# Kernel optimization log

Measured on AMD Instinct MI355X. Metric: run time of the kernel, lower is better.

The kernel has to match this reference:

```python
import jax, jax.numpy as jnp
import numpy as np

N, E, IN, HID, H, HD, PE_D, D, L = 50000, 800000, 128, 64, 4, 16, 16, 16, 2
BN_S = 1.0 / np.sqrt(1.0 + 1e-5)  # eval-mode BatchNorm1d with default running stats (mean=0, var=1)
SCALE = 1.0 / np.sqrt(HD)         # np.sqrt(self.out_dim) with out_dim = head_dim


def _ln(x, g, b, eps=1e-5):
    mu = jnp.mean(x, -1, keepdims=True)
    v = jnp.mean((x - mu) ** 2, -1, keepdims=True)
    return (x - mu) * jax.lax.rsqrt(v + eps) * g + b


def setup_inputs() -> dict:
    key = jax.random.key(0)
    ks = iter(jax.random.split(key, 64))

    def nrm(shape, s=0.05):
        return jax.random.normal(next(ks), shape, jnp.float32) * s

    return {
        'src': jax.random.randint(next(ks), (E,), 0, N),
        'dst': jnp.sort(jax.random.randint(next(ks), (E,), 0, N)),
        'x': nrm((N, IN), 1.0), 'pe': nrm((N, PE_D), 1.0),
        'de': nrm((E, D), 1.0), 'm': nrm((E, 8), 1.0), 'I': nrm((N, D), 1.0),
        'W_h': nrm((IN, HID)),
        'W_pe': nrm((PE_D, HID)), 'b_pe': jnp.zeros((HID,)),
        'W_de': nrm((D, HID)), 'b_de': jnp.zeros((HID,)),
        'W_m': nrm((8, HID)), 'b_m': jnp.zeros((HID,)),
        'Wq': nrm((L, HID, HID)), 'bq': jnp.zeros((L, HID)),
        'Wk': nrm((L, HID, HID)), 'bk': jnp.zeros((L, HID)),
        'Wv': nrm((L, HID, HID)), 'bv': jnp.zeros((L, HID)),
        'Wpd': nrm((L, HID, HID)), 'bpd': jnp.zeros((L, HID)),
        'Wpm': nrm((L, HID, HID)), 'bpm': jnp.zeros((L, HID)),
        'WO': nrm((L, HID, HID)), 'bO': jnp.zeros((L, HID)),
        'Wpi': nrm((L, D, HID)), 'bpi': jnp.zeros((L, HID)),
        'g1': jnp.ones((L, HID)), 'b1': jnp.zeros((L, HID)),
        'g2': jnp.ones((L, HID)), 'b2': jnp.zeros((L, HID)),
        'Wf1': nrm((L, HID, 2 * HID)), 'bf1': jnp.zeros((L, 2 * HID)),
        'Wf2': nrm((L, 2 * HID, HID)), 'bf2': jnp.zeros((L, HID)),
        'Wr1': nrm((HID, 16)), 'br1': jnp.zeros((16,)),
        'Wr2': nrm((16, IN)), 'br2': jnp.zeros((IN,)),
    }


def _forward(src, dst, x, pe, de, m, I, W_h, W_pe, b_pe, W_de, b_de, W_m, b_m,
             Wq, bq, Wk, bk, Wv, bv, Wpd, bpd, Wpm, bpm, WO, bO, Wpi, bpi,
             g1, b1, g2, b2, Wf1, bf1, Wf2, bf2, Wr1, br1, Wr2, br2):
    h = x @ W_h + pe @ W_pe + b_pe          # [N, HID]
    m_e = m @ W_m + b_m                     # [E, HID]
    de_e = de @ W_de + b_de                 # [E, HID]
    for l in range(L):
        h_in1 = h
        Qh = (h @ Wq[l] + bq[l]).reshape(N, H, HD)
        Kh = (h @ Wk[l] + bk[l]).reshape(N, H, HD)
        Vh = (h @ Wv[l] + bv[l]).reshape(N, H, HD)
        pd = (de_e @ Wpd[l] + bpd[l]).reshape(E, H, HD)
        pm = (m_e @ Wpm[l] + bpm[l]).reshape(E, H, HD)
        # edge scores: src_dot_dst -> scale -> + proj_d -> + proj_m -> exp(clamped sum)
        s = jnp.sum(Kh[src] * Qh[dst], -1, keepdims=True) * SCALE   # [E, H, 1]
        s = jnp.sum(s + pd + pm, -1, keepdims=True)                 # [E, H, 1]
        s = jnp.exp(jnp.clip(s, -5.0, 5.0))
        # scatter-sum message passing to destination nodes
        wV = jax.ops.segment_sum(Vh[src] * s, dst, num_segments=N, indices_are_sorted=True)
        z = jax.ops.segment_sum(s, dst, num_segments=N, indices_are_sorted=True)
        h = (wV / (z + 1e-10)).reshape(N, HID)
        h = h + I @ Wpi[l] + bpi[l]          # dropout is identity in eval
        h = h @ WO[l] + bO[l]
        h = h_in1 + h
        h = _ln(h, g1[l], b1[l]) * BN_S      # LayerNorm then eval BatchNorm
        h_in2 = h
        h2 = jax.nn.relu(h @ Wf1[l] + bf1[l]) @ Wf2[l] + bf2[l]
        h = _ln(h_in2 + h2, g2[l], b2[l]) * BN_S
    x_hat = jax.nn.selu(h @ Wr1 + br1) @ Wr2 + br2
    return h, x_hat


def reference(src, dst, x, pe, de, m, I, W_h, W_pe, b_pe, W_de, b_de, W_m, b_m,
              Wq, bq, Wk, bk, Wv, bv, Wpd, bpd, Wpm, bpm, WO, bO, Wpi, bpi,
              g1, b1, g2, b2, Wf1, bf1, Wf2, bf2, Wr1, br1, Wr2, br2):
    return _forward(src, dst, x, pe, de, m, I, W_h, W_pe, b_pe, W_de, b_de, W_m, b_m,
                    Wq, bq, Wk, bk, Wv, bv, Wpd, bpd, Wpm, bpm, WO, bO, Wpi, bpi,
                    g1, b1, g2, b2, Wf1, bf1, Wf2, bf2, Wr1, br1, Wr2, br2)
```

## Files before the change

### kernel.cpp

```cpp
#include <hip/hip_runtime.h>
#include <hip/hip_bf16.h>

typedef __hip_bfloat16 bf16;
typedef __attribute__((ext_vector_type(8))) short s8v;
typedef __attribute__((ext_vector_type(4))) float f4v;
typedef __attribute__((ext_vector_type(8))) _Float16 h8v;
#define DEV __device__ __forceinline__
#define MFMA(a, b, c) __builtin_amdgcn_mfma_f32_16x16x32_bf16(a, b, c, 0, 0, 0)

constexpr int OFF_WQ = 0, OFF_WK = 8192, OFF_WV = 16384, OFF_WO = 24576;
constexpr int OFF_WF1 = 32768, OFF_WF2 = 49152, OFF_WPI = 65536;
constexpr int PL = 69632;
constexpr int OFF_WH = 139264, OFF_WPE = 155648, OFF_WR1 = 159744, OFF_WR2 = 161792;
constexpr int WBF_TOT = 169984;

constexpr float LOG2E = 1.4426950408889634f;
constexpr float QSC = 4.f * LOG2E;
constexpr float CLB = 5.f * LOG2E;

DEV short f2bs(float f) { union { bf16 b; short s; } u; u.b = __float2bfloat16(f); return u.s; }
DEV float bs2f(short s) { union { bf16 b; short s2; } u; u.s2 = s; return __bfloat162float(u.b); }
DEV ushort f2hs(float f) { union { _Float16 h; ushort u; } x; x.h = (_Float16)f; return x.u; }

DEV void split8(const float* p, s8v& hi, s8v& lo) {
  #pragma unroll
  for (int j = 0; j < 8; ++j) {
    float f = p[j];
    short h = f2bs(f);
    hi[j] = h;
    lo[j] = f2bs(f - bs2f(h));
  }
}

__global__ __launch_bounds__(256) void prep_kernel(
    const float* __restrict__ Wq, const float* __restrict__ Wk,
    const float* __restrict__ Wv, const float* __restrict__ WO,
    const float* __restrict__ Wf1, const float* __restrict__ Wf2,
    const float* __restrict__ Wpi, const float* __restrict__ W_h,
    const float* __restrict__ W_pe, const float* __restrict__ Wr1,
    const float* __restrict__ Wr2, short* __restrict__ wb)
{
  const float* sp; int K, ksh, Nc, d0;
  switch (blockIdx.y) {
    case 0:  sp = Wq;         K = 64;  ksh = 6; Nc = 64;  d0 = OFF_WQ;       break;
    case 1:  sp = Wk;         K = 64;  ksh = 6; Nc = 64;  d0 = OFF_WK;       break;
    case 2:  sp = Wv;         K = 64;  ksh = 6; Nc = 64;  d0 = OFF_WV;       break;
    case 3:  sp = WO;         K = 64;  ksh = 6; Nc = 64;  d0 = OFF_WO;       break;
    case 4:  sp = Wf1;        K = 64;  ksh = 6; Nc = 128; d0 = OFF_WF1;      break;
    case 5:  sp = Wf2;        K = 128; ksh = 7; Nc = 64;  d0 = OFF_WF2;      break;
    case 6:  sp = Wpi;        K = 16;  ksh = 5; Nc = 64;  d0 = OFF_WPI;      break;
    case 7:  sp = Wq + 4096;  K = 64;  ksh = 6; Nc = 64;  d0 = PL + OFF_WQ;  break;
    case 8:  sp = Wk + 4096;  K = 64;  ksh = 6; Nc = 64;  d0 = PL + OFF_WK;  break;
    case 9:  sp = Wv + 4096;  K = 64;  ksh = 6; Nc = 64;  d0 = PL + OFF_WV;  break;
    case 10: sp = WO + 4096;  K = 64;  ksh = 6; Nc = 64;  d0 = PL + OFF_WO;  break;
    case 11: sp = Wf1 + 8192; K = 64;  ksh = 6; Nc = 128; d0 = PL + OFF_WF1; break;
    case 12: sp = Wf2 + 8192; K = 128; ksh = 7; Nc = 64;  d0 = PL + OFF_WF2; break;
    case 13: sp = Wpi + 1024; K = 16;  ksh = 5; Nc = 64;  d0 = PL + OFF_WPI; break;
    case 14: sp = W_h;        K = 128; ksh = 7; Nc = 64;  d0 = OFF_WH;       break;
    case 15: sp = W_pe;       K = 16;  ksh = 5; Nc = 64;  d0 = OFF_WPE;      break;
    case 16: sp = Wr1;        K = 64;  ksh = 6; Nc = 16;  d0 = OFF_WR1;      break;
    default: sp = Wr2;        K = 16;  ksh = 5; Nc = 128; d0 = OFF_WR2;      break;
  }
  int Kp = 1 << ksh;
  int tot = Kp * Nc;
  int i = blockIdx.x * 256 + threadIdx.x;
  if (i >= tot) return;
  int o = i >> ksh, kk = i & (Kp - 1);
  float v = (kk < K) ? sp[kk * Nc + o] : 0.f;
  short h = f2bs(v);
  wb[d0 + i] = h;
  wb[d0 + tot + i] = f2bs(v - bs2f(h));
}

__global__ __launch_bounds__(256) void fold_kernel(
    const float* __restrict__ W_de, const float* __restrict__ b_de,
    const float* __restrict__ W_m,  const float* __restrict__ b_m,
    const float* __restrict__ Wpd,  const float* __restrict__ bpd,
    const float* __restrict__ Wpm,  const float* __restrict__ bpm,
    float* __restrict__ fold)
{
  __shared__ float spd[64][4], spm[64][4];
  int tid = threadIdx.x;
  for (int l = 0; l < 2; ++l) {
    {
      int t = tid >> 2, hh = tid & 3;
      const float* wpd = Wpd + l * 4096 + t * 64 + hh * 16;
      const float* wpm = Wpm + l * 4096 + t * 64 + hh * 16;
      float sd = 0.f, sm = 0.f;
      #pragma unroll
      for (int hd = 0; hd < 16; ++hd) { sd += wpd[hd]; sm += wpm[hd]; }
      spd[t][hh] = sd; spm[t][hh] = sm;
    }
    __syncthreads();
    if (tid < 64) { int i = tid >> 2, hh = tid & 3;
      float a = 0.f;
      for (int k = 0; k < 64; ++k) a += W_de[i * 64 + k] * spd[k][hh];
      fold[l * 128 + i * 4 + hh] = a; }
    if (tid < 32) { int i = tid >> 2, hh = tid & 3;
      float a = 0.f;
      for (int k = 0; k < 64; ++k) a += W_m[i * 64 + k] * spm[k][hh];
      fold[l * 128 + 64 + i * 4 + hh] = a; }
    if (tid < 4) { int hh = tid;
      float a = 0.f;
      for (int k = 0; k < 64; ++k) a += b_de[k] * spd[k][hh] + b_m[k] * spm[k][hh];
      for (int hd = 0; hd < 16; ++hd)
        a += bpd[l * 64 + hh * 16 + hd] + bpm[l * 64 + hh * 16 + hd];
      fold[l * 128 + 96 + hh] = a; }
    __syncthreads();
  }
}

__global__ __launch_bounds__(256) void escore_kernel(
    const float* __restrict__ de, const float* __restrict__ m,
    const float* __restrict__ fold, ushort* __restrict__ ep0,
    ushort* __restrict__ ep1, int E, int lay)
{
  int e = blockIdx.x * 256 + threadIdx.x;
  if (e >= E) return;
  float dv[16], mv[8];
  #pragma unroll
  for (int i = 0; i < 4; ++i)
    *(float4*)(dv + 4 * i) = ((const float4*)(de + (size_t)e * 16))[i];
  #pragma unroll
  for (int i = 0; i < 2; ++i)
    *(float4*)(mv + 4 * i) = ((const float4*)(m + (size_t)e * 8))[i];
  #pragma unroll
  for (int pass = 0; pass < 2; ++pass) {
    ushort* ep; int l;
    if (pass == 0) { ep = ep0; l = ep1 ? 0 : lay; }
    else { if (!ep1) break; ep = ep1; l = 1; }
    const float* f = fold + l * 128;
    ushort4 o;
    ushort* op = (ushort*)&o;
    #pragma unroll
    for (int hh = 0; hh < 4; ++hh) {
      float a = f[96 + hh];
      #pragma unroll
      for (int i = 0; i < 16; ++i) a += dv[i] * f[i * 4 + hh];
      #pragma unroll
      for (int i = 0; i < 8; ++i) a += mv[i] * f[64 + i * 4 + hh];
      op[hh] = f2hs(a * LOG2E);
    }
    *(ushort4*)(ep + (size_t)e * 4) = o;
  }
}

__global__ __launch_bounds__(256) void rowptr_kernel(
    const int* __restrict__ dst, int E, int N, int* __restrict__ rp)
{
  int n = blockIdx.x * blockDim.x + threadIdx.x;
  if (n > N) return;
  int lo = 0, hi = E;
  while (lo < hi) {
    int mid = (lo + hi) >> 1;
    if (dst[mid] < n) lo = mid + 1; else hi = mid;
  }
  rp[n] = lo;
}

__global__ __launch_bounds__(256) void hinit_mfma(
    const float* __restrict__ x, const float* __restrict__ pe,
    const short* __restrict__ wb, const float* __restrict__ b_pe,
    ushort* __restrict__ Hb, int N)
{
  __shared__ __align__(16) ushort sH[64][72];
  int tid = threadIdx.x, wv = tid >> 6, ln = tid & 63;
  int q = ln >> 4, p16 = ln & 15;
  int nb0 = blockIdx.x * 64;
  int arow = nb0 + wv * 16 + p16; if (arow >= N) arow = N - 1;
  f4v acc[4] = {};
  for (int kt = 0; kt < 4; ++kt) {
    s8v ah, al;
    split8(x + (size_t)arow * 128 + kt * 32 + 8 * q, ah, al);
    #pragma unroll
    for (int ct = 0; ct < 4; ++ct) {
      int bo = (ct * 16 + p16) * 128 + kt * 32 + 8 * q;
      s8v bh = *(const s8v*)(wb + OFF_WH + bo);
      s8v bl = *(const s8v*)(wb + OFF_WH + 8192 + bo);
      acc[ct] = MFMA(ah, bh, acc[ct]);
      acc[ct] = MFMA(ah, bl, acc[ct]);
      acc[ct] = MFMA(al, bh, acc[ct]);
    }
  }
  {
    s8v ah = {}, al = {};
    if (q < 2) split8(pe + (size_t)arow * 16 + 8 * q, ah, al);
    #pragma unroll
    for (int ct = 0; ct < 4; ++ct) {
      int bo = (ct * 16 + p16) * 32 + 8 * q;
      s8v bh = *(const s8v*)(wb + OFF_WPE + bo);
      s8v bl = *(const s8v*)(wb + OFF_WPE + 2048 + bo);
      acc[ct] = MFMA(ah, bh, acc[ct]);
      acc[ct] = MFMA(ah, bl, acc[ct]);
      acc[ct] = MFMA(al, bh, acc[ct]);
    }
  }
  #pragma unroll
  for (int ct = 0; ct < 4; ++ct) {
    float bb = b_pe[ct * 16 + p16];
    #pragma unroll
    for (int j = 0; j < 4; ++j)
      sH[wv * 16 + q * 4 + j][ct * 16 + p16] = (ushort)f2bs(acc[ct][j] + bb);
  }
  __syncthreads();
  int row = tid >> 2, part = tid & 3;
  if (nb0 + row < N) {
    uint4 a0 = *(uint4*)&sH[row][part * 16];
    uint4 a1 = *(uint4*)&sH[row][part * 16 + 8];
    *(uint4*)(Hb + (size_t)(nb0 + row) * 64 + part * 16) = a0;
    *(uint4*)(Hb + (size_t)(nb0 + row) * 64 + part * 16 + 8) = a1;
  }
}

__global__ __launch_bounds__(256) void qkv_mfma(
    const ushort* __restrict__ Hb, const short* __restrict__ wb,
    const float* __restrict__ bq, const float* __restrict__ bk, const float* __restrict__ bv,
    float* __restrict__ Qb, ushort* __restrict__ Kb, ushort* __restrict__ Vb,
    int N, int lay)
{
  __shared__ __align__(16) ushort sK[64][72];
  __shared__ __align__(16) ushort sV[64][72];
  int tid = threadIdx.x, wv = tid >> 6, ln = tid & 63;
  int q = ln >> 4, p16 = ln & 15;
  int nb0 = blockIdx.x * 64;
  int arow = nb0 + wv * 16 + p16; if (arow >= N) arow = N - 1;
  int wbase = lay * PL;
  s8v a0 = *(const s8v*)(Hb + (size_t)arow * 64 + 8 * q);
  s8v a1 = *(const s8v*)(Hb + (size_t)arow * 64 + 32 + 8 * q);
  f4v qa[4] = {}, ka[4] = {}, va[4] = {};
  #pragma unroll
  for (int kt = 0; kt < 2; ++kt) {
    s8v a = kt ? a1 : a0;
    #pragma unroll
    for (int ct = 0; ct < 4; ++ct) {
      int bo = (ct * 16 + p16) * 64 + kt * 32 + 8 * q;
      s8v bh, bl;
      bh = *(const s8v*)(wb + wbase + OFF_WQ + bo);
      bl = *(const s8v*)(wb + wbase + OFF_WQ + 4096 + bo);
      qa[ct] = MFMA(a, bh, qa[ct]); qa[ct] = MFMA(a, bl, qa[ct]);
      bh = *(const s8v*)(wb + wbase + OFF_WK + bo);
      bl = *(const s8v*)(wb + wbase + OFF_WK + 4096 + bo);
      ka[ct] = MFMA(a, bh, ka[ct]); ka[ct] = MFMA(a, bl, ka[ct]);
      bh = *(const s8v*)(wb + wbase + OFF_WV + bo);
      bl = *(const s8v*)(wb + wbase + OFF_WV + 4096 + bo);
      va[ct] = MFMA(a, bh, va[ct]); va[ct] = MFMA(a, bl, va[ct]);
    }
  }
  #pragma unroll
  for (int ct = 0; ct < 4; ++ct) {
    int col = ct * 16 + p16;
    float bQ = bq[lay * 64 + col], bK = bk[lay * 64 + col], bV = bv[lay * 64 + col];
    #pragma unroll
    for (int j = 0; j < 4; ++j) {
      int r = nb0 + wv * 16 + q * 4 + j;
      if (r < N) Qb[(size_t)r * 64 + col] = (qa[ct][j] + bQ) * QSC;
      sK[wv * 16 + q * 4 + j][col] = f2hs(ka[ct][j] + bK);
      sV[wv * 16 + q * 4 + j][col] = f2hs(va[ct][j] + bV);
    }
  }
  __syncthreads();
  int row = tid >> 2, part = tid & 3;
  if (nb0 + row < N) {
    uint4 k0 = *(uint4*)&sK[row][part * 16];
    uint4 k1 = *(uint4*)&sK[row][part * 16 + 8];
    *(uint4*)(Kb + (size_t)(nb0 + row) * 64 + part * 16) = k0;
    *(uint4*)(Kb + (size_t)(nb0 + row) * 64 + part * 16 + 8) = k1;
    uint4 v0 = *(uint4*)&sV[row][part * 16];
    uint4 v1 = *(uint4*)&sV[row][part * 16 + 8];
    *(uint4*)(Vb + (size_t)(nb0 + row) * 64 + part * 16) = v0;
    *(uint4*)(Vb + (size_t)(nb0 + row) * 64 + part * 16 + 8) = v1;
  }
}

__global__ __launch_bounds__(256, 4) void edge_kernel(
    const float* __restrict__ Qb, const _Float16* __restrict__ Kb,
    const _Float16* __restrict__ Vb, const int* __restrict__ src,
    const int* __restrict__ rp, const _Float16* __restrict__ epsl,
    ushort* __restrict__ attnb, int N)
{
  __shared__ float red[4][16][64];
  int tid = threadIdx.x, ln = tid & 63;
  int wv = __builtin_amdgcn_readfirstlane(tid >> 6);
  int w = blockIdx.x * 4 + wv;
  bool wok = w < N;
  int wc = wok ? w : N - 1;
  int es = ln >> 2, h = ln & 3;

  float q[16];
  const float* qp = Qb + (size_t)wc * 64 + h * 16;
  #pragma unroll
  for (int i = 0; i < 4; ++i)
    *(float4*)(q + 4 * i) = ((const float4*)qp)[i];

  int e0 = rp[wc], e1 = rp[wc + 1];
  int elast = e1 - 1;
  float acc[16];
  #pragma unroll
  for (int i = 0; i < 16; ++i) acc[i] = 0.f;
  float z = 0.f;

  for (int e = e0; e < e1; e += 16) {
    int eidx = e + es;
    bool val = eidx <= elast;
    int eic = val ? eidx : elast;
    int sidx = src[eic];
    size_t ko = (size_t)sidx * 64 + h * 16;
    h8v k0 = *(const h8v*)(Kb + ko);
    h8v k1 = *(const h8v*)(Kb + ko + 8);
    h8v v0 = *(const h8v*)(Vb + ko);
    h8v v1 = *(const h8v*)(Vb + ko + 8);
    float pe_ = (float)epsl[(size_t)eic * 4 + h];
    float t0 = 0.f, t1 = 0.f;
    #pragma unroll
    for (int i = 0; i < 8; ++i) {
      t0 = fmaf((float)k0[i], q[i], t0);
      t1 = fmaf((float)k1[i], q[i + 8], t1);
    }
    float sc = fminf(fmaxf(t0 + t1 + pe_, -CLB), CLB);
    float sv = __builtin_amdgcn_exp2f(sc);
    sv = val ? sv : 0.f;
    z += sv;
    #pragma unroll
    for (int i = 0; i < 8; ++i) {
      acc[i] = fmaf(sv, (float)v0[i], acc[i]);
      acc[i + 8] = fmaf(sv, (float)v1[i], acc[i + 8]);
    }
  }

  z += __shfl_xor(z, 4, 64);
  z += __shfl_xor(z, 8, 64);
  z += __shfl_xor(z, 16, 64);
  z += __shfl_xor(z, 32, 64);

  float* rw = &red[wv][es][h * 16];
  #pragma unroll
  for (int i = 0; i < 4; ++i)
    *(float4*)(rw + i * 4) = *(const float4*)(acc + i * 4);
  __asm__ volatile("s_waitcnt lgkmcnt(0)" ::: "memory");
  int c = ln;
  float zc = __shfl(z, c >> 4, 64);
  float s = 0.f;
  #pragma unroll
  for (int es2 = 0; es2 < 16; ++es2) s += red[wv][es2][c];
  if (wok) attnb[(size_t)w * 64 + c] = (ushort)f2bs(s / (zc + 1e-10f));
}

__global__ __launch_bounds__(256) void post_mfma(
    ushort* __restrict__ Hb, const ushort* __restrict__ attnb,
    const float* __restrict__ I, const short* __restrict__ wb,
    const float* __restrict__ bpi, const float* __restrict__ bO,
    const float* __restrict__ g1, const float* __restrict__ b1,
    const float* __restrict__ bf1, const float* __restrict__ bf2,
    const float* __restrict__ g2, const float* __restrict__ b2,
    int N, int lay)
{
  constexpr float BN_S = 0.9999950000374997f;
  __shared__ __align__(16) ushort sH[64][72];
  __shared__ __align__(16) ushort sA[64][72];
  __shared__ float sF[64][65];
  __shared__ __align__(16) ushort sT[64][136];
  int tid = threadIdx.x, wv = tid >> 6, ln = tid & 63;
  int q = ln >> 4, p16 = ln & 15;
  int nb0 = blockIdx.x * 64;
  {
    int row = tid >> 2, part = tid & 3;
    int gr = nb0 + row; if (gr >= N) gr = N - 1;
    uint4 h0 = *(const uint4*)(Hb + (size_t)gr * 64 + part * 16);
    uint4 h1 = *(const uint4*)(Hb + (size_t)gr * 64 + part * 16 + 8);
    *(uint4*)&sH[row][part * 16] = h0;
    *(uint4*)&sH[row][part * 16 + 8] = h1;
    uint4 t0 = *(const uint4*)(attnb + (size_t)gr * 64 + part * 16);
    uint4 t1 = *(const uint4*)(attnb + (size_t)gr * 64 + part * 16 + 8);
    *(uint4*)&sA[row][part * 16] = t0;
    *(uint4*)&sA[row][part * 16 + 8] = t1;
  }
  __syncthreads();
  int wbase = lay * PL;
  int arow = nb0 + wv * 16 + p16; if (arow >= N) arow = N - 1;
  f4v uacc[4] = {};
  {
    s8v ah = {}, al = {};
    if (q < 2) split8(I + (size_t)arow * 16 + 8 * q, ah, al);
    #pragma unroll
    for (int ct = 0; ct < 4; ++ct) {
      int bo = (ct * 16 + p16) * 32 + 8 * q;
      s8v bh = *(const s8v*)(wb + wbase + OFF_WPI + bo);
      s8v bl = *(const s8v*)(wb + wbase + OFF_WPI + 2048 + bo);
      uacc[ct] = MFMA(ah, bh, uacc[ct]);
      uacc[ct] = MFMA(ah, bl, uacc[ct]);
      uacc[ct] = MFMA(al, bh, uacc[ct]);
    }
  }
  #pragma unroll
  for (int ct = 0; ct < 4; ++ct) {
    int col = ct * 16 + p16;
    float bb = bpi[lay * 64 + col];
    #pragma unroll
    for (int j = 0; j < 4; ++j) {
      uacc[ct][j] += bb + bs2f((short)sA[wv * 16 + q * 4 + j][col]);
      sF[wv * 16 + q * 4 + j][col] = uacc[ct][j];
    }
  }
  __syncthreads();
  f4v vacc[4] = {};
  #pragma unroll
  for (int kt = 0; kt < 2; ++kt) {
    s8v ah, al;
    split8(&sF[wv * 16 + p16][kt * 32 + 8 * q], ah, al);
    #pragma unroll
    for (int ct = 0; ct < 4; ++ct) {
      int bo = (ct * 16 + p16) * 64 + kt * 32 + 8 * q;
      s8v bh = *(const s8v*)(wb + wbase + OFF_WO + bo);
      s8v bl = *(const s8v*)(wb + wbase + OFF_WO + 4096 + bo);
      vacc[ct] = MFMA(ah, bh, vacc[ct]);
      vacc[ct] = MFMA(ah, bl, vacc[ct]);
      vacc[ct] = MFMA(al, bh, vacc[ct]);
    }
  }
  float hw[4][4];
  #pragma unroll
  for (int ct = 0; ct < 4; ++ct) {
    int col = ct * 16 + p16;
    float bb = bO[lay * 64 + col];
    #pragma unroll
    for (int j = 0; j < 4; ++j)
      hw[ct][j] = bs2f((short)sH[wv * 16 + q * 4 + j][col]) + vacc[ct][j] + bb;
  }
  float h1r[4][4];
  {
    float s0[4], mu[4], vv[4], rs[4];
    #pragma unroll
    for (int j = 0; j < 4; ++j) s0[j] = hw[0][j] + hw[1][j] + hw[2][j] + hw[3][j];
    #pragma unroll
    for (int msk = 1; msk < 16; msk <<= 1)
      #pragma unroll
      for (int j = 0; j < 4; ++j) s0[j] += __shfl_xor(s0[j], msk, 64);
    #pragma unroll
    for (int j = 0; j < 4; ++j) { mu[j] = s0[j] * (1.f / 64.f); vv[j] = 0.f; }
    #pragma unroll
    for (int ct = 0; ct < 4; ++ct)
      #pragma unroll
      for (int j = 0; j < 4; ++j) { float d = hw[ct][j] - mu[j]; hw[ct][j] = d; vv[j] += d * d; }
    #pragma unroll
    for (int msk = 1; msk < 16; msk <<= 1)
      #pragma unroll
      for (int j = 0; j < 4; ++j) vv[j] += __shfl_xor(vv[j], msk, 64);
    #pragma unroll
    for (int j = 0; j < 4; ++j) rs[j] = 1.f / sqrtf(vv[j] * (1.f / 64.f) + 1e-5f);
    #pragma unroll
    for (int ct = 0; ct < 4; ++ct) {
      int col = ct * 16 + p16;
      float gg = g1[lay * 64 + col], bb = b1[lay * 64 + col];
      #pragma unroll
      for (int j = 0; j < 4; ++j)
        h1r[ct][j] = (hw[ct][j] * rs[j] * gg + bb) * BN_S;
    }
  }
  __syncthreads();
  #pragma unroll
  for (int ct = 0; ct < 4; ++ct)
    #pragma unroll
    for (int j = 0; j < 4; ++j)
      sF[wv * 16 + q * 4 + j][ct * 16 + p16] = h1r[ct][j];
  __syncthreads();
  f4v tacc[8] = {};
  #pragma unroll
  for (int kt = 0; kt < 2; ++kt) {
    s8v ah, al;
    split8(&sF[wv * 16 + p16][kt * 32 + 8 * q], ah, al);
    #pragma unroll
    for (int ct = 0; ct < 8; ++ct) {
      int bo = (ct * 16 + p16) * 64 + kt * 32 + 8 * q;
      s8v bh = *(const s8v*)(wb + wbase + OFF_WF1 + bo);
      s8v bl = *(const s8v*)(wb + wbase + OFF_WF1 + 8192 + bo);
      tacc[ct] = MFMA(ah, bh, tacc[ct]);
      tacc[ct] = MFMA(ah, bl, tacc[ct]);
      tacc[ct] = MFMA(al, bh, tacc[ct]);
    }
  }
  #pragma unroll
  for (int ct = 0; ct < 8; ++ct) {
    int col = ct * 16 + p16;
    float bb = bf1[lay * 128 + col];
    #pragma unroll
    for (int j = 0; j < 4; ++j)
      sT[wv * 16 + q * 4 + j][col] = (ushort)f2bs(fmaxf(tacc[ct][j] + bb, 0.f));
  }
  __syncthreads();
  f4v yacc[4] = {};
  #pragma unroll
  for (int kt = 0; kt < 4; ++kt) {
    s8v at = *(const s8v*)&sT[wv * 16 + p16][kt * 32 + 8 * q];
    #pragma unroll
    for (int ct = 0; ct < 4; ++ct) {
      int bo = (ct * 16 + p16) * 128 + kt * 32 + 8 * q;
      s8v bh = *(const s8v*)(wb + wbase + OFF_WF2 + bo);
      s8v bl = *(const s8v*)(wb + wbase + OFF_WF2 + 8192 + bo);
      yacc[ct] = MFMA(at, bh, yacc[ct]);
      yacc[ct] = MFMA(at, bl, yacc[ct]);
    }
  }
  float w2[4][4];
  #pragma unroll
  for (int ct = 0; ct < 4; ++ct) {
    int col = ct * 16 + p16;
    float bb = bf2[lay * 64 + col];
    #pragma unroll
    for (int j = 0; j < 4; ++j)
      w2[ct][j] = h1r[ct][j] + yacc[ct][j] + bb;
  }
  {
    float s0[4], mu[4], vv[4], rs[4];
    #pragma unroll
    for (int j = 0; j < 4; ++j) s0[j] = w2[0][j] + w2[1][j] + w2[2][j] + w2[3][j];
    #pragma unroll
    for (int msk = 1; msk < 16; msk <<= 1)
      #pragma unroll
      for (int j = 0; j < 4; ++j) s0[j] += __shfl_xor(s0[j], msk, 64);
    #pragma unroll
    for (int j = 0; j < 4; ++j) { mu[j] = s0[j] * (1.f / 64.f); vv[j] = 0.f; }
    #pragma unroll
    for (int ct = 0; ct < 4; ++ct)
      #pragma unroll
      for (int j = 0; j < 4; ++j) { float d = w2[ct][j] - mu[j]; w2[ct][j] = d; vv[j] += d * d; }
    #pragma unroll
    for (int msk = 1; msk < 16; msk <<= 1)
      #pragma unroll
      for (int j = 0; j < 4; ++j) vv[j] += __shfl_xor(vv[j], msk, 64);
    #pragma unroll
    for (int j = 0; j < 4; ++j) rs[j] = 1.f / sqrtf(vv[j] * (1.f / 64.f) + 1e-5f);
    #pragma unroll
    for (int ct = 0; ct < 4; ++ct) {
      int col = ct * 16 + p16;
      float gg = g2[lay * 64 + col], bb = b2[lay * 64 + col];
      #pragma unroll
      for (int j = 0; j < 4; ++j)
        sH[wv * 16 + q * 4 + j][col] = (ushort)f2bs((w2[ct][j] * rs[j] * gg + bb) * BN_S);
    }
  }
  __syncthreads();
  {
    int row = tid >> 2, part = tid & 3;
    if (nb0 + row < N) {
      uint4 a0 = *(uint4*)&sH[row][part * 16];
      uint4 a1 = *(uint4*)&sH[row][part * 16 + 8];
      *(uint4*)(Hb + (size_t)(nb0 + row) * 64 + part * 16) = a0;
      *(uint4*)(Hb + (size_t)(nb0 + row) * 64 + part * 16 + 8) = a1;
    }
  }
}

__global__ __launch_bounds__(256) void readout_mfma(
    const ushort* __restrict__ Hb, const short* __restrict__ wb,
    const float* __restrict__ br1, const float* __restrict__ br2,
    float* __restrict__ out, int N)
{
  __shared__ __align__(16) ushort sH[64][72];
  __shared__ float sM[64][17];
  int tid = threadIdx.x, wv = tid >> 6, ln = tid & 63;
  int q = ln >> 4, p16 = ln & 15;
  int nb0 = blockIdx.x * 64;
  {
    int row = tid >> 2, part = tid & 3;
    int gr = nb0 + row; if (gr >= N) gr = N - 1;
    uint4 h0 = *(const uint4*)(Hb + (size_t)gr * 64 + part * 16);
    uint4 h1 = *(const uint4*)(Hb + (size_t)gr * 64 + part * 16 + 8);
    *(uint4*)&sH[row][part * 16] = h0;
    *(uint4*)&sH[row][part * 16 + 8] = h1;
  }
  __syncthreads();
  {
    int row = tid >> 2, part = tid & 3;
    if (nb0 + row < N) {
      #pragma unroll
      for (int c = 0; c < 16; ++c)
        out[(size_t)(nb0 + row) * 64 + part * 16 + c] = bs2f((short)sH[row][part * 16 + c]);
    }
  }
  f4v macc = {};
  #pragma unroll
  for (int kt = 0; kt < 2; ++kt) {
    s8v a = *(const s8v*)&sH[wv * 16 + p16][kt * 32 + 8 * q];
    int bo = p16 * 64 + kt * 32 + 8 * q;
    s8v bh = *(const s8v*)(wb + OFF_WR1 + bo);
    s8v bl = *(const s8v*)(wb + OFF_WR1 + 1024 + bo);
    macc = MFMA(a, bh, macc);
    macc = MFMA(a, bl, macc);
  }
  const float SC = 1.0507009873554805f, AL = 1.6732632423543772f;
  #pragma unroll
  for (int j = 0; j < 4; ++j) {
    float md = macc[j] + br1[p16];
    md = (md > 0.f) ? SC * md : SC * AL * expm1f(md);
    sM[wv * 16 + q * 4 + j][p16] = md;
  }
  __syncthreads();
  f4v xacc[8] = {};
  {
    s8v ah = {}, al = {};
    if (q < 2) split8(&sM[wv * 16 + p16][8 * q], ah, al);
    #pragma unroll
    for (int ct = 0; ct < 8; ++ct) {
      int bo = (ct * 16 + p16) * 32 + 8 * q;
      s8v bh = *(const s8v*)(wb + OFF_WR2 + bo);
      s8v bl = *(const s8v*)(wb + OFF_WR2 + 4096 + bo);
      xacc[ct] = MFMA(ah, bh, xacc[ct]);
      xacc[ct] = MFMA(ah, bl, xacc[ct]);
      xacc[ct] = MFMA(al, bh, xacc[ct]);
    }
  }
  #pragma unroll
  for (int ct = 0; ct < 8; ++ct) {
    int col = ct * 16 + p16;
    float bb = br2[col];
    #pragma unroll
    for (int j = 0; j < 4; ++j) {
      int r = nb0 + wv * 16 + q * 4 + j;
      if (r < N) out[(size_t)N * 64 + (size_t)r * 128 + col] = xacc[ct][j] + bb;
    }
  }
}

extern "C" void kernel_launch(void* const* d_in, const int* in_sizes, int n_in,
                              void* d_out, int out_size, void* d_ws, size_t ws_size,
                              hipStream_t stream)
{
  const int* src    = (const int*)d_in[0];
  const int* dst    = (const int*)d_in[1];
  const float* x    = (const float*)d_in[2];
  const float* pe   = (const float*)d_in[3];
  const float* de   = (const float*)d_in[4];
  const float* m    = (const float*)d_in[5];
  const float* I    = (const float*)d_in[6];
  const float* W_h  = (const float*)d_in[7];
  const float* W_pe = (const float*)d_in[8];
  const float* b_pe = (const float*)d_in[9];
  const float* W_de = (const float*)d_in[10];
  const float* b_de = (const float*)d_in[11];
  const float* W_m  = (const float*)d_in[12];
  const float* b_m  = (const float*)d_in[13];
  const float* Wq   = (const float*)d_in[14];
  const float* bq   = (const float*)d_in[15];
  const float* Wk   = (const float*)d_in[16];
  const float* bk   = (const float*)d_in[17];
  const float* Wv   = (const float*)d_in[18];
  const float* bv   = (const float*)d_in[19];
  const float* Wpd  = (const float*)d_in[20];
  const float* bpd  = (const float*)d_in[21];
  const float* Wpm  = (const float*)d_in[22];
  const float* bpm  = (const float*)d_in[23];
  const float* WO   = (const float*)d_in[24];
  const float* bO   = (const float*)d_in[25];
  const float* Wpi  = (const float*)d_in[26];
  const float* bpi  = (const float*)d_in[27];
  const float* g1   = (const float*)d_in[28];
  const float* b1   = (const float*)d_in[29];
  const float* g2   = (const float*)d_in[30];
  const float* b2   = (const float*)d_in[31];
  const float* Wf1  = (const float*)d_in[32];
  const float* bf1  = (const float*)d_in[33];
  const float* Wf2  = (const float*)d_in[34];
  const float* bf2  = (const float*)d_in[35];
  const float* Wr1  = (const float*)d_in[36];
  const float* br1  = (const float*)d_in[37];
  const float* Wr2  = (const float*)d_in[38];
  const float* br2  = (const float*)d_in[39];

  const int E = in_sizes[0];
  const int N = in_sizes[2] / 128;

  char* ws = (char*)d_ws;
  int* row_ptr = (int*)ws;
  size_t rp_bytes = (((size_t)(N + 1) * 4) + 255) & ~(size_t)255;
  float* fold = (float*)(ws + rp_bytes);
  short* wb = (short*)(ws + rp_bytes + 1024);
  ushort* Hb = (ushort*)(ws + rp_bytes + 1024 + (size_t)WBF_TOT * 2);
  size_t ws_used = rp_bytes + 1024 + (size_t)WBF_TOT * 2 + (size_t)N * 128;

  float* out = (float*)d_out;
  ushort* Kb = (ushort*)out;
  ushort* Vb = Kb + (size_t)N * 64;
  float* Qb = out + (size_t)N * 64;
  ushort* attnb = (ushort*)((char*)d_out + (size_t)N * 512);

  bool both_eps = ws_size >= ws_used + (size_t)E * 16;
  ushort *eps0, *eps1 = nullptr;
  if (both_eps) {
    eps0 = (ushort*)(ws + ws_used);
    eps1 = eps0 + (size_t)E * 4;
  } else {
    eps0 = (ushort*)((char*)d_out + (size_t)N * 640);
  }

  int nb64 = (N + 63) / 64;

  prep_kernel<<<dim3(32, 18), 256, 0, stream>>>(Wq, Wk, Wv, WO, Wf1, Wf2, Wpi,
                                                W_h, W_pe, Wr1, Wr2, wb);
  fold_kernel<<<1, 256, 0, stream>>>(W_de, b_de, W_m, b_m, Wpd, bpd, Wpm, bpm, fold);
  rowptr_kernel<<<(N + 256) / 256, 256, 0, stream>>>(dst, E, N, row_ptr);
  hinit_mfma<<<nb64, 256, 0, stream>>>(x, pe, wb, b_pe, Hb, N);
  if (both_eps)
    escore_kernel<<<(E + 255) / 256, 256, 0, stream>>>(de, m, fold, eps0, eps1, E, 0);

  for (int lay = 0; lay < 2; ++lay) {
    if (!both_eps)
      escore_kernel<<<(E + 255) / 256, 256, 0, stream>>>(de, m, fold, eps0, nullptr, E, lay);
    qkv_mfma<<<nb64, 256, 0, stream>>>(Hb, wb, bq, bk, bv, Qb, Kb, Vb, N, lay);
    edge_kernel<<<(N + 3) / 4, 256, 0, stream>>>(Qb, (const _Float16*)Kb,
        (const _Float16*)Vb, src, row_ptr,
        (const _Float16*)((both_eps && lay) ? eps1 : eps0), attnb, N);
    post_mfma<<<nb64, 256, 0, stream>>>(Hb, attnb, I, wb, bpi, bO, g1, b1,
                                        bf1, bf2, g2, b2, N, lay);
  }
  readout_mfma<<<nb64, 256, 0, stream>>>(Hb, wb, br1, br2, out, N);
}
```

Before: 502.4 us.

## Fuse QKV projection into hinit and post kernels, use per-wave LDS without barriers

Merges the standalone QKV projection into the H-init kernel and into the tail of the layer-0 post kernel, so the two qkv_mfma launches and their re-read of Hb disappear. Shared-memory staging is replaced by per-wave private buffers, which removes all __syncthreads. Post and readout kernels now load H and attention rows directly into registers. The cost is that the coalesced 16-byte row stores through LDS become scattered 2- or 4-byte global stores, and register pressure in the fused post kernel goes up.

```diff
diff --git a/kernel.cpp b/kernel.cpp
--- a/kernel.cpp
+++ b/kernel.cpp
@@ -158,16 +158,21 @@
   rp[n] = lo;
 }
 
-__global__ __launch_bounds__(256) void hinit_mfma(
+__global__ __launch_bounds__(256) void hinit_qkv(
     const float* __restrict__ x, const float* __restrict__ pe,
     const short* __restrict__ wb, const float* __restrict__ b_pe,
-    ushort* __restrict__ Hb, int N)
-{
-  __shared__ __align__(16) ushort sH[64][72];
+    const float* __restrict__ bq, const float* __restrict__ bk,
+    const float* __restrict__ bv, ushort* __restrict__ Hb,
+    float* __restrict__ Qb, ushort* __restrict__ Kb, ushort* __restrict__ Vb,
+    int N)
+{
+  __shared__ __align__(16) char bufc[4][4352];
   int tid = threadIdx.x, wv = tid >> 6, ln = tid & 63;
   int q = ln >> 4, p16 = ln & 15;
   int nb0 = blockIdx.x * 64;
   int arow = nb0 + wv * 16 + p16; if (arow >= N) arow = N - 1;
+  ushort* bu = (ushort*)bufc[wv];
+
   f4v acc[4] = {};
   for (int kt = 0; kt < 4; ++kt) {
     s8v ah, al;
@@ -195,38 +200,21 @@
       acc[ct] = MFMA(al, bh, acc[ct]);
     }
   }
+  int rb = nb0 + wv * 16 + q * 4;
   #pragma unroll
   for (int ct = 0; ct < 4; ++ct) {
-    float bb = b_pe[ct * 16 + p16];
-    #pragma unroll
-    for (int j = 0; j < 4; ++j)
-      sH[wv * 16 + q * 4 + j][ct * 16 + p16] = (ushort)f2bs(acc[ct][j] + bb);
-  }
-  __syncthreads();
-  int row = tid >> 2, part = tid & 3;
-  if (nb0 + row < N) {
-    uint4 a0 = *(uint4*)&sH[row][part * 16];
-    uint4 a1 = *(uint4*)&sH[row][part * 16 + 8];
-    *(uint4*)(Hb + (size_t)(nb0 + row) * 64 + part * 16) = a0;
-    *(uint4*)(Hb + (size_t)(nb0 + row) * 64 + part * 16 + 8) = a1;
-  }
-}
-
-__global__ __launch_bounds__(256) void qkv_mfma(
-    const ushort* __restrict__ Hb, const short* __restrict__ wb,
-    const float* __restrict__ bq, const float* __restrict__ bk, const float* __restrict__ bv,
-    float* __restrict__ Qb, ushort* __restrict__ Kb, ushort* __restrict__ Vb,
-    int N, int lay)
-{
-  __shared__ __align__(16) ushort sK[64][72];
-  __shared__ __align__(16) ushort sV[64][72];
-  int tid = threadIdx.x, wv = tid >> 6, ln = tid & 63;
-  int q = ln >> 4, p16 = ln & 15;
-  int nb0 = blockIdx.x * 64;
-  int arow = nb0 + wv * 16 + p16; if (arow >= N) arow = N - 1;
-  int wbase = lay * PL;
-  s8v a0 = *(const s8v*)(Hb + (size_t)arow * 64 + 8 * q);
-  s8v a1 = *(const s8v*)(Hb + (size_t)arow * 64 + 32 + 8 * q);
+    int col = ct * 16 + p16;
+    float bb = b_pe[col];
+    #pragma unroll
+    for (int j = 0; j < 4; ++j) {
+      ushort hv = (ushort)f2bs(acc[ct][j] + bb);
+      bu[(q * 4 + j) * 72 + col] = hv;
+      if (rb + j < N) Hb[(size_t)(rb + j) * 64 + col] = hv;
+    }
+  }
+  s8v a0 = *(const s8v*)&bu[p16 * 72 + 8 * q];
+  s8v a1 = *(const s8v*)&bu[p16 * 72 + 32 + 8 * q];
+
   f4v qa[4] = {}, ka[4] = {}, va[4] = {};
   #pragma unroll
   for (int kt = 0; kt < 2; ++kt) {
@@ -235,40 +223,30 @@
     for (int ct = 0; ct < 4; ++ct) {
       int bo = (ct * 16 + p16) * 64 + kt * 32 + 8 * q;
       s8v bh, bl;
-      bh = *(const s8v*)(wb + wbase + OFF_WQ + bo);
-      bl = *(const s8v*)(wb + wbase + OFF_WQ + 4096 + bo);
+      bh = *(const s8v*)(wb + OFF_WQ + bo);
+      bl = *(const s8v*)(wb + OFF_WQ + 4096 + bo);
       qa[ct] = MFMA(a, bh, qa[ct]); qa[ct] = MFMA(a, bl, qa[ct]);
-      bh = *(const s8v*)(wb + wbase + OFF_WK + bo);
-      bl = *(const s8v*)(wb + wbase + OFF_WK + 4096 + bo);
+      bh = *(const s8v*)(wb + OFF_WK + bo);
+      bl = *(const s8v*)(wb + OFF_WK + 4096 + bo);
       ka[ct] = MFMA(a, bh, ka[ct]); ka[ct] = MFMA(a, bl, ka[ct]);
-      bh = *(const s8v*)(wb + wbase + OFF_WV + bo);
-      bl = *(const s8v*)(wb + wbase + OFF_WV + 4096 + bo);
+      bh = *(const s8v*)(wb + OFF_WV + bo);
+      bl = *(const s8v*)(wb + OFF_WV + 4096 + bo);
       va[ct] = MFMA(a, bh, va[ct]); va[ct] = MFMA(a, bl, va[ct]);
     }
   }
   #pragma unroll
   for (int ct = 0; ct < 4; ++ct) {
     int col = ct * 16 + p16;
-    float bQ = bq[lay * 64 + col], bK = bk[lay * 64 + col], bV = bv[lay * 64 + col];
+    float bQ = bq[col], bK = bk[col], bV = bv[col];
     #pragma unroll
     for (int j = 0; j < 4; ++j) {
-      int r = nb0 + wv * 16 + q * 4 + j;
-      if (r < N) Qb[(size_t)r * 64 + col] = (qa[ct][j] + bQ) * QSC;
-      sK[wv * 16 + q * 4 + j][col] = f2hs(ka[ct][j] + bK);
-      sV[wv * 16 + q * 4 + j][col] = f2hs(va[ct][j] + bV);
-    }
-  }
-  __syncthreads();
-  int row = tid >> 2, part = tid & 3;
-  if (nb0 + row < N) {
-    uint4 k0 = *(uint4*)&sK[row][part * 16];
-    uint4 k1 = *(uint4*)&sK[row][part * 16 + 8];
-    *(uint4*)(Kb + (size_t)(nb0 + row) * 64 + part * 16) = k0;
-    *(uint4*)(Kb + (size_t)(nb0 + row) * 64 + part * 16 + 8) = k1;
-    uint4 v0 = *(uint4*)&sV[row][part * 16];
-    uint4 v1 = *(uint4*)&sV[row][part * 16 + 8];
-    *(uint4*)(Vb + (size_t)(nb0 + row) * 64 + part * 16) = v0;
-    *(uint4*)(Vb + (size_t)(nb0 + row) * 64 + part * 16 + 8) = v1;
+      if (rb + j < N) {
+        size_t o = (size_t)(rb + j) * 64 + col;
+        Qb[o] = (qa[ct][j] + bQ) * QSC;
+        Kb[o] = f2hs(ka[ct][j] + bK);
+        Vb[o] = f2hs(va[ct][j] + bV);
+      }
+    }
   }
 }
 
@@ -345,38 +323,42 @@
   if (wok) attnb[(size_t)w * 64 + c] = (ushort)f2bs(s / (zc + 1e-10f));
 }
 
-__global__ __launch_bounds__(256) void post_mfma(
+template<int TAIL>
+__global__ __launch_bounds__(256) void post_fused(
     ushort* __restrict__ Hb, const ushort* __restrict__ attnb,
     const float* __restrict__ I, const short* __restrict__ wb,
     const float* __restrict__ bpi, const float* __restrict__ bO,
     const float* __restrict__ g1, const float* __restrict__ b1,
     const float* __restrict__ bf1, const float* __restrict__ bf2,
     const float* __restrict__ g2, const float* __restrict__ b2,
-    int N, int lay)
+    const float* __restrict__ bq, const float* __restrict__ bk,
+    const float* __restrict__ bv, float* __restrict__ Qb,
+    ushort* __restrict__ Kb, ushort* __restrict__ Vb, int N, int lay)
 {
   constexpr float BN_S = 0.9999950000374997f;
-  __shared__ __align__(16) ushort sH[64][72];
-  __shared__ __align__(16) ushort sA[64][72];
-  __shared__ float sF[64][65];
-  __shared__ __align__(16) ushort sT[64][136];
+  __shared__ __align__(16) char bufc[4][4352];
   int tid = threadIdx.x, wv = tid >> 6, ln = tid & 63;
   int q = ln >> 4, p16 = ln & 15;
   int nb0 = blockIdx.x * 64;
-  {
-    int row = tid >> 2, part = tid & 3;
-    int gr = nb0 + row; if (gr >= N) gr = N - 1;
-    uint4 h0 = *(const uint4*)(Hb + (size_t)gr * 64 + part * 16);
-    uint4 h1 = *(const uint4*)(Hb + (size_t)gr * 64 + part * 16 + 8);
-    *(uint4*)&sH[row][part * 16] = h0;
-    *(uint4*)&sH[row][part * 16 + 8] = h1;
-    uint4 t0 = *(const uint4*)(attnb + (size_t)gr * 64 + part * 16);
-    uint4 t1 = *(const uint4*)(attnb + (size_t)gr * 64 + part * 16 + 8);
-    *(uint4*)&sA[row][part * 16] = t0;
-    *(uint4*)&sA[row][part * 16 + 8] = t1;
-  }
-  __syncthreads();
   int wbase = lay * PL;
+  int rb = nb0 + wv * 16 + q * 4;
+  int r_[4];
+  #pragma unroll
+  for (int j = 0; j < 4; ++j) { int rr = rb + j; r_[j] = (rr < N) ? rr : N - 1; }
+
+  float hC[4][4], aC[4][4];
+  #pragma unroll
+  for (int j = 0; j < 4; ++j) {
+    const ushort* hp = Hb + (size_t)r_[j] * 64 + p16;
+    const ushort* ap = attnb + (size_t)r_[j] * 64 + p16;
+    #pragma unroll
+    for (int ct = 0; ct < 4; ++ct) {
+      hC[ct][j] = bs2f((short)hp[ct * 16]);
+      aC[ct][j] = bs2f((short)ap[ct * 16]);
+    }
+  }
   int arow = nb0 + wv * 16 + p16; if (arow >= N) arow = N - 1;
+
   f4v uacc[4] = {};
   {
     s8v ah = {}, al = {};
@@ -391,22 +373,20 @@
       uacc[ct] = MFMA(al, bh, uacc[ct]);
     }
   }
+  float* bf = (float*)bufc[wv];
   #pragma unroll
   for (int ct = 0; ct < 4; ++ct) {
     int col = ct * 16 + p16;
     float bb = bpi[lay * 64 + col];
     #pragma unroll
-    for (int j = 0; j < 4; ++j) {
-      uacc[ct][j] += bb + bs2f((short)sA[wv * 16 + q * 4 + j][col]);
-      sF[wv * 16 + q * 4 + j][col] = uacc[ct][j];
-    }
-  }
-  __syncthreads();
+    for (int j = 0; j < 4; ++j)
+      bf[(q * 4 + j) * 68 + col] = uacc[ct][j] + bb + aC[ct][j];
+  }
   f4v vacc[4] = {};
   #pragma unroll
   for (int kt = 0; kt < 2; ++kt) {
     s8v ah, al;
-    split8(&sF[wv * 16 + p16][kt * 32 + 8 * q], ah, al);
+    split8(&bf[p16 * 68 + kt * 32 + 8 * q], ah, al);
     #pragma unroll
     for (int ct = 0; ct < 4; ++ct) {
       int bo = (ct * 16 + p16) * 64 + kt * 32 + 8 * q;
@@ -424,7 +404,7 @@
     float bb = bO[lay * 64 + col];
     #pragma unroll
     for (int j = 0; j < 4; ++j)
-      hw[ct][j] = bs2f((short)sH[wv * 16 + q * 4 + j][col]) + vacc[ct][j] + bb;
+      hw[ct][j] = hC[ct][j] + vacc[ct][j] + bb;
   }
   float h1r[4][4];
   {
@@ -456,18 +436,16 @@
         h1r[ct][j] = (hw[ct][j] * rs[j] * gg + bb) * BN_S;
     }
   }
-  __syncthreads();
   #pragma unroll
   for (int ct = 0; ct < 4; ++ct)
     #pragma unroll
     for (int j = 0; j < 4; ++j)
-      sF[wv * 16 + q * 4 + j][ct * 16 + p16] = h1r[ct][j];
-  __syncthreads();
+      bf[(q * 4 + j) * 68 + ct * 16 + p16] = h1r[ct][j];
   f4v tacc[8] = {};
   #pragma unroll
   for (int kt = 0; kt < 2; ++kt) {
     s8v ah, al;
-    split8(&sF[wv * 16 + p16][kt * 32 + 8 * q], ah, al);
+    split8(&bf[p16 * 68 + kt * 32 + 8 * q], ah, al);
     #pragma unroll
     for (int ct = 0; ct < 8; ++ct) {
       int bo = (ct * 16 + p16) * 64 + kt * 32 + 8 * q;
@@ -478,19 +456,19 @@
       tacc[ct] = MFMA(al, bh, tacc[ct]);
     }
   }
+  ushort* bu = (ushort*)bufc[wv];
   #pragma unroll
   for (int ct = 0; ct < 8; ++ct) {
     int col = ct * 16 + p16;
     float bb = bf1[lay * 128 + col];
     #pragma unroll
     for (int j = 0; j < 4; ++j)
-      sT[wv * 16 + q * 4 + j][col] = (ushort)f2bs(fmaxf(tacc[ct][j] + bb, 0.f));
-  }
-  __syncthreads();
+      bu[(q * 4 + j) * 136 + col] = (ushort)f2bs(fmaxf(tacc[ct][j] + bb, 0.f));
+  }
   f4v yacc[4] = {};
   #pragma unroll
   for (int kt = 0; kt < 4; ++kt) {
-    s8v at = *(const s8v*)&sT[wv * 16 + p16][kt * 32 + 8 * q];
+    s8v at = *(const s8v*)&bu[p16 * 136 + kt * 32 + 8 * q];
     #pragma unroll
     for (int ct = 0; ct < 4; ++ct) {
       int bo = (ct * 16 + p16) * 128 + kt * 32 + 8 * q;
@@ -509,6 +487,7 @@
     for (int j = 0; j < 4; ++j)
       w2[ct][j] = h1r[ct][j] + yacc[ct][j] + bb;
   }
+  ushort h2b[4][4];
   {
     float s0[4], mu[4], vv[4], rs[4];
     #pragma unroll
@@ -535,52 +514,103 @@
       float gg = g2[lay * 64 + col], bb = b2[lay * 64 + col];
       #pragma unroll
       for (int j = 0; j < 4; ++j)
-        sH[wv * 16 + q * 4 + j][col] = (ushort)f2bs((w2[ct][j] * rs[j] * gg + bb) * BN_S);
-    }
-  }
-  __syncthreads();
-  {
-    int row = tid >> 2, part = tid & 3;
-    if (nb0 + row < N) {
-      uint4 a0 = *(uint4*)&sH[row][part * 16];
-      uint4 a1 = *(uint4*)&sH[row][part * 16 + 8];
-      *(uint4*)(Hb + (size_t)(nb0 + row) * 64 + part * 16) = a0;
-      *(uint4*)(Hb + (size_t)(nb0 + row) * 64 + part * 16 + 8) = a1;
-    }
-  }
-}
-
-__global__ __launch_bounds__(256) void readout_mfma(
+        h2b[ct][j] = (ushort)f2bs((w2[ct][j] * rs[j] * gg + bb) * BN_S);
+    }
+  }
+  #pragma unroll
+  for (int ct = 0; ct < 4; ++ct) {
+    int col = ct * 16 + p16;
+    #pragma unroll
+    for (int j = 0; j < 4; ++j)
+      if (rb + j < N) Hb[(size_t)(rb + j) * 64 + col] = h2b[ct][j];
+  }
+  if (TAIL) {
+    #pragma unroll
+    for (int ct = 0; ct < 4; ++ct)
+      #pragma unroll
+      for (int j = 0; j < 4; ++j)
+        bu[(q * 4 + j) * 72 + ct * 16 + p16] = h2b[ct][j];
+    s8v a0 = *(const s8v*)&bu[p16 * 72 + 8 * q];
+    s8v a1 = *(const s8v*)&bu[p16 * 72 + 32 + 8 * q];
+    int wb2 = (lay + 1) * PL;
+    f4v qa[4] = {}, ka[4] = {}, va[4] = {};
+    #pragma unroll
+    for (int kt = 0; kt < 2; ++kt) {
+      s8v a = kt ? a1 : a0;
+      #pragma unroll
+      for (int ct = 0; ct < 4; ++ct) {
+        int bo = (ct * 16 + p16) * 64 + kt * 32 + 8 * q;
+        s8v bh, bl;
+        bh = *(const s8v*)(wb + wb2 + OFF_WQ + bo);
+        bl = *(const s8v*)(wb + wb2 + OFF_WQ + 4096 + bo);
+        qa[ct] = MFMA(a, bh, qa[ct]); qa[ct] = MFMA(a, bl, qa[ct]);
+        bh = *(const s8v*)(wb + wb2 + OFF_WK + bo);
+        bl = *(const s8v*)(wb + wb2 + OFF_WK + 4096 + bo);
+        ka[ct] = MFMA(a, bh, ka[ct]); ka[ct] = MFMA(a, bl, ka[ct]);
+        bh = *(const s8v*)(wb + wb2 + OFF_WV + bo);
+        bl = *(const s8v*)(wb + wb2 + OFF_WV + 4096 + bo);
+        va[ct] = MFMA(a, bh, va[ct]); va[ct] = MFMA(a, bl, va[ct]);
+      }
+    }
+    #pragma unroll
+    for (int ct = 0; ct < 4; ++ct) {
+      int col = ct * 16 + p16;
+      float bQ = bq[(lay + 1) * 64 + col];
+      float bK = bk[(lay + 1) * 64 + col];
+      float bV = bv[(lay + 1) * 64 + col];
+      #pragma unroll
+      for (int j = 0; j < 4; ++j) {
+        if (rb + j < N) {
+          size_t o = (size_t)(rb + j) * 64 + col;
+          Qb[o] = (qa[ct][j] + bQ) * QSC;
+          Kb[o] = f2hs(ka[ct][j] + bK);
+          Vb[o] = f2hs(va[ct][j] + bV);
+        }
+      }
+    }
+  }
+}
+
+__global__ __launch_bounds__(256) void readout_f(
     const ushort* __restrict__ Hb, const short* __restrict__ wb,
     const float* __restrict__ br1, const float* __restrict__ br2,
     float* __restrict__ out, int N)
 {
-  __shared__ __align__(16) ushort sH[64][72];
-  __shared__ float sM[64][17];
+  __shared__ __align__(16) char bufc[4][4352];
   int tid = threadIdx.x, wv = tid >> 6, ln = tid & 63;
   int q = ln >> 4, p16 = ln & 15;
   int nb0 = blockIdx.x * 64;
-  {
-    int row = tid >> 2, part = tid & 3;
-    int gr = nb0 + row; if (gr >= N) gr = N - 1;
-    uint4 h0 = *(const uint4*)(Hb + (size_t)gr * 64 + part * 16);
-    uint4 h1 = *(const uint4*)(Hb + (size_t)gr * 64 + part * 16 + 8);
-    *(uint4*)&sH[row][part * 16] = h0;
-    *(uint4*)&sH[row][part * 16 + 8] = h1;
-  }
-  __syncthreads();
-  {
-    int row = tid >> 2, part = tid & 3;
-    if (nb0 + row < N) {
-      #pragma unroll
-      for (int c = 0; c < 16; ++c)
-        out[(size_t)(nb0 + row) * 64 + part * 16 + c] = bs2f((short)sH[row][part * 16 + c]);
-    }
-  }
+  int rb = nb0 + wv * 16 + q * 4;
+  int r_[4];
+  #pragma unroll
+  for (int j = 0; j < 4; ++j) { int rr = rb + j; r_[j] = (rr < N) ? rr : N - 1; }
+
+  ushort hC[4][4];
+  #pragma unroll
+  for (int j = 0; j < 4; ++j) {
+    const ushort* hp = Hb + (size_t)r_[j] * 64 + p16;
+    #pragma unroll
+    for (int ct = 0; ct < 4; ++ct) hC[ct][j] = hp[ct * 16];
+  }
+  #pragma unroll
+  for (int ct = 0; ct < 4; ++ct) {
+    int col = ct * 16 + p16;
+    #pragma unroll
+    for (int j = 0; j < 4; ++j)
+      if (rb + j < N) out[(size_t)(rb + j) * 64 + col] = bs2f((short)hC[ct][j]);
+  }
+  ushort* bu = (ushort*)bufc[wv];
+  #pragma unroll
+  for (int ct = 0; ct < 4; ++ct)
+    #pragma unroll
+    for (int j = 0; j < 4; ++j)
+      bu[(q * 4 + j) * 72 + ct * 16 + p16] = hC[ct][j];
+  s8v a0 = *(const s8v*)&bu[p16 * 72 + 8 * q];
+  s8v a1 = *(const s8v*)&bu[p16 * 72 + 32 + 8 * q];
   f4v macc = {};
   #pragma unroll
   for (int kt = 0; kt < 2; ++kt) {
-    s8v a = *(const s8v*)&sH[wv * 16 + p16][kt * 32 + 8 * q];
+    s8v a = kt ? a1 : a0;
     int bo = p16 * 64 + kt * 32 + 8 * q;
     s8v bh = *(const s8v*)(wb + OFF_WR1 + bo);
     s8v bl = *(const s8v*)(wb + OFF_WR1 + 1024 + bo);
@@ -588,36 +618,33 @@
     macc = MFMA(a, bl, macc);
   }
   const float SC = 1.0507009873554805f, AL = 1.6732632423543772f;
+  float* bf = (float*)bufc[wv];
   #pragma unroll
   for (int j = 0; j < 4; ++j) {
     float md = macc[j] + br1[p16];
     md = (md > 0.f) ? SC * md : SC * AL * expm1f(md);
-    sM[wv * 16 + q * 4 + j][p16] = md;
-  }
-  __syncthreads();
+    bf[(q * 4 + j) * 24 + p16] = md;
+  }
+  s8v ah = {}, al = {};
+  if (q < 2) split8(&bf[p16 * 24 + 8 * q], ah, al);
   f4v xacc[8] = {};
-  {
-    s8v ah = {}, al = {};
-    if (q < 2) split8(&sM[wv * 16 + p16][8 * q], ah, al);
-    #pragma unroll
-    for (int ct = 0; ct < 8; ++ct) {
-      int bo = (ct * 16 + p16) * 32 + 8 * q;
-      s8v bh = *(const s8v*)(wb + OFF_WR2 + bo);
-      s8v bl = *(const s8v*)(wb + OFF_WR2 + 4096 + bo);
-      xacc[ct] = MFMA(ah, bh, xacc[ct]);
-      xacc[ct] = MFMA(ah, bl, xacc[ct]);
-      xacc[ct] = MFMA(al, bh, xacc[ct]);
-    }
-  }
   #pragma unroll
   for (int ct = 0; ct < 8; ++ct) {
+    int bo = (ct * 16 + p16) * 32 + 8 * q;
+    s8v bh = *(const s8v*)(wb + OFF_WR2 + bo);
+    s8v bl = *(const s8v*)(wb + OFF_WR2 + 4096 + bo);
+    xacc[ct] = MFMA(ah, bh, xacc[ct]);
+    xacc[ct] = MFMA(ah, bl, xacc[ct]);
+    xacc[ct] = MFMA(al, bh, xacc[ct]);
+  }
+  #pragma unroll
+  for (int ct = 0; ct < 8; ++ct) {
     int col = ct * 16 + p16;
     float bb = br2[col];
     #pragma unroll
-    for (int j = 0; j < 4; ++j) {
-      int r = nb0 + wv * 16 + q * 4 + j;
-      if (r < N) out[(size_t)N * 64 + (size_t)r * 128 + col] = xacc[ct][j] + bb;
-    }
+    for (int j = 0; j < 4; ++j)
+      if (rb + j < N)
+        out[(size_t)N * 64 + (size_t)(rb + j) * 128 + col] = xacc[ct][j] + bb;
   }
 }
 
@@ -698,19 +725,23 @@
                                                 W_h, W_pe, Wr1, Wr2, wb);
   fold_kernel<<<1, 256, 0, stream>>>(W_de, b_de, W_m, b_m, Wpd, bpd, Wpm, bpm, fold);
   rowptr_kernel<<<(N + 256) / 256, 256, 0, stream>>>(dst, E, N, row_ptr);
-  hinit_mfma<<<nb64, 256, 0, stream>>>(x, pe, wb, b_pe, Hb, N);
   if (both_eps)
     escore_kernel<<<(E + 255) / 256, 256, 0, stream>>>(de, m, fold, eps0, eps1, E, 0);
+
+  hinit_qkv<<<nb64, 256, 0, stream>>>(x, pe, wb, b_pe, bq, bk, bv, Hb, Qb, Kb, Vb, N);
 
   for (int lay = 0; lay < 2; ++lay) {
     if (!both_eps)
       escore_kernel<<<(E + 255) / 256, 256, 0, stream>>>(de, m, fold, eps0, nullptr, E, lay);
-    qkv_mfma<<<nb64, 256, 0, stream>>>(Hb, wb, bq, bk, bv, Qb, Kb, Vb, N, lay);
     edge_kernel<<<(N + 3) / 4, 256, 0, stream>>>(Qb, (const _Float16*)Kb,
         (const _Float16*)Vb, src, row_ptr,
         (const _Float16*)((both_eps && lay) ? eps1 : eps0), attnb, N);
-    post_mfma<<<nb64, 256, 0, stream>>>(Hb, attnb, I, wb, bpi, bO, g1, b1,
-                                        bf1, bf2, g2, b2, N, lay);
-  }
-  readout_mfma<<<nb64, 256, 0, stream>>>(Hb, wb, br1, br2, out, N);
-}
+    if (lay == 0)
+      post_fused<1><<<nb64, 256, 0, stream>>>(Hb, attnb, I, wb, bpi, bO, g1, b1,
+          bf1, bf2, g2, b2, bq, bk, bv, Qb, Kb, Vb, N, 0);
+    else
+      post_fused<0><<<nb64, 256, 0, stream>>>(Hb, attnb, I, wb, bpi, bO, g1, b1,
+          bf1, bf2, g2, b2, bq, bk, bv, Qb, Kb, Vb, N, 1);
+  }
+  readout_f<<<nb64, 256, 0, stream>>>(Hb, wb, br1, br2, out, N);
+}
```

Measured after the change: 488.5 us. 2.8% less time.
